# Performance work log

Hardware: AMD Instinct MI355X
Metric: run time of the kernel (lower is better)

Reference implementation:

```python
import jax, jax.numpy as jnp
import numpy as np

B, T, E = 512, 12, 1024   # batch, channels/seq, embed_dim
NH, HS = 8, 128           # num_heads, head_size (head_size=128 hard-coded in source)
H = NH * HS               # sLSTM hidden = 1024 (== E)


def _layer_norm(x, g, b, eps=1e-5):
    mu = x.mean(-1, keepdims=True)
    var = x.var(-1, keepdims=True)
    return (x - mu) * jax.lax.rsqrt(var + eps) * g + b


def _conv1d_same(x, w, b):
    # x: (B, C, L), w: (O, I, K) odd K, 'same' padding, stride 1
    k = w.shape[-1]
    p = (k - 1) // 2
    y = jax.lax.conv_general_dilated(x, w, (1,), [(p, p)],
                                     dimension_numbers=('NCH', 'OIH', 'NCH'))
    return y + b[None, :, None]


def setup_inputs():
    key = jax.random.key(0)
    ks = jax.random.split(key, 16)
    s = 0.02
    def nrm(k, shape, scale=s):
        return jax.random.normal(k, shape, jnp.float32) * scale
    return {
        'x': jax.random.normal(ks[0], (B, T, E), jnp.float32),
        'ln_g': jnp.ones((E,), jnp.float32), 'ln_b': jnp.zeros((E,), jnp.float32),
        'fc1_w': nrm(ks[1], (12, 12, 3)), 'fc1_b': jnp.zeros((12,), jnp.float32),
        'fc2_w': nrm(ks[2], (12, 12)), 'fc2_b': jnp.zeros((12,), jnp.float32),
        'conv1_w': nrm(ks[3], (48, 12, 3)), 'conv1_b': jnp.zeros((48,), jnp.float32),
        'conv2_w': nrm(ks[4], (12, 48, 3)), 'conv2_b': jnp.zeros((12,), jnp.float32),
        'xl_ln_g': jnp.ones((E,), jnp.float32), 'xl_ln_b': jnp.zeros((E,), jnp.float32),
        'Wg': nrm(ks[5], (E, 4 * H)), 'bg': jnp.zeros((4 * H,), jnp.float32),
        'Rg': nrm(ks[6], (NH, 4 * HS, HS)),
        'gn_g': jnp.ones((H,), jnp.float32), 'gn_b': jnp.zeros((H,), jnp.float32),
        'upl_w': nrm(ks[7], (H, H)), 'upl_b': jnp.zeros((H,), jnp.float32),
        'upr_w': nrm(ks[8], (H, H)), 'upr_b': jnp.zeros((H,), jnp.float32),
        'down_w': nrm(ks[9], (H, E)), 'down_b': jnp.zeros((E,), jnp.float32),
    }


def _slstm_block(x, xl_ln_g, xl_ln_b, Wg, bg, Rg, gn_g, gn_b,
                 upl_w, upl_b, upr_w, upr_b, down_w, down_b):
    # Stabilized multi-head sLSTM block: pre-LN -> sLSTM recurrence (exp i/f gates
    # with max-stabilizer m), per-head GroupNorm, gated up/down proj (proj_factor=1),
    # residual. Recurrent weights are block-diagonal per head (NH, 4*HS, HS).
    xn = _layer_norm(x, xl_ln_g, xl_ln_b)
    gx = jnp.einsum('bte,eg->btg', xn, Wg) + bg            # (B,T,4H) input gate pre-acts
    gx = jnp.swapaxes(gx, 0, 1)                            # (T,B,4H)

    def step(carry, g_t):
        h, c, n, m = carry                                 # each (B,NH,HS)
        rec = jnp.einsum('bnh,ngh->bng', h, Rg)            # (B,NH,4HS)
        g = g_t.reshape(g_t.shape[0], NH, 4 * HS) + rec
        z_, i_, f_, o_ = jnp.split(g, 4, axis=-1)
        z = jnp.tanh(z_)
        o = jax.nn.sigmoid(o_)
        m_new = jnp.maximum(f_ + m, i_)                    # log-space stabilizer
        i = jnp.exp(i_ - m_new)
        f = jnp.exp(f_ + m - m_new)
        c = f * c + i * z
        n = f * n + i
        h = o * (c / n)
        return (h, c, n, m_new), h

    zero = jnp.zeros((x.shape[0], NH, HS), x.dtype)
    _, hseq = jax.lax.scan(step, (zero, zero, zero, zero), gx)
    h = jnp.swapaxes(hseq, 0, 1)                           # (B,T,NH,HS)
    # GroupNorm(num_groups=NH) over each head's HS channels
    mu = h.mean(-1, keepdims=True)
    var = h.var(-1, keepdims=True)
    hn = (h - mu) * jax.lax.rsqrt(var + 1e-5)
    hn = hn.reshape(x.shape[0], x.shape[1], H) * gn_g + gn_b
    left = jax.nn.gelu(hn @ upl_w + upl_b, approximate=False)
    right = hn @ upr_w + upr_b
    return (left * right) @ down_w + down_b + x


def reference(x, ln_g, ln_b, fc1_w, fc1_b, fc2_w, fc2_b, conv1_w, conv1_b,
              conv2_w, conv2_b, xl_ln_g, xl_ln_b, Wg, bg, Rg, gn_g, gn_b,
              upl_w, upl_b, upr_w, upr_b, down_w, down_b):
    xn = _layer_norm(x, ln_g, ln_b)
    skip = xn
    xc = _conv1d_same(xn, fc1_w, fc1_b)                    # fc1: Conv1d(12,12,3,'same')
    x1 = jnp.einsum('bcl,oc->bol', xc, fc2_w) + fc2_b[None, :, None]  # fc2: 1x1 conv
    x1 = _slstm_block(x1, xl_ln_g, xl_ln_b, Wg, bg, Rg, gn_g, gn_b,
                      upl_w, upl_b, upr_w, upr_b, down_w, down_b)
    # dropout(0.2) is identity in eval mode
    y = jax.nn.silu(xc) * x1 + skip
    z = _conv1d_same(y, conv1_w, conv1_b)                  # 12 -> 48
    z = _layer_norm(jax.nn.gelu(z, approximate=False), ln_g, ln_b)
    z = _conv1d_same(z, conv2_w, conv2_b)                  # 48 -> 12
    return z + skip
```

## Files before the change

### kernel.cpp

```cpp
#include <hip/hip_runtime.h>
#include <math.h>


typedef short short8_t __attribute__((ext_vector_type(8)));
typedef float floatx4 __attribute__((ext_vector_type(4)));
typedef float float2_t __attribute__((ext_vector_type(2)));

typedef unsigned int u32;
typedef const __attribute__((address_space(1))) u32 gu32;
typedef __attribute__((address_space(3))) u32 lu32;

static __device__ __forceinline__ float b2f(unsigned short u) {
    unsigned v = ((unsigned)u) << 16;
    return __builtin_bit_cast(float, v);
}
static __device__ __forceinline__ unsigned short f2b(float f) {
    unsigned u = __builtin_bit_cast(unsigned, f);
    u += 0x7FFFu + ((u >> 16) & 1u);
    return (unsigned short)(u >> 16);
}
static __device__ __forceinline__ float2_t make2u(unsigned u) {
    float2_t r;
    r.x = __builtin_bit_cast(float, u << 16);
    r.y = __builtin_bit_cast(float, u & 0xFFFF0000u);
    return r;
}
static __device__ __forceinline__ u32 pack2(float a, float b) {
    return ((u32)f2b(b) << 16) | (u32)f2b(a);
}
static __device__ __forceinline__ float gelu_fast(float x) {
    float u = 0.7978845608f * x * (1.f + 0.044715f * x * x);
    u = fminf(fmaxf(u, -9.f), 9.f);
    return x * __builtin_amdgcn_rcpf(1.f + __expf(-2.f * u));
}


__global__ __launch_bounds__(256) void transpose_bf16_k(
    const float* __restrict__ src, unsigned short* __restrict__ dst, int K, int N)
{
    __shared__ unsigned short tl[32][33];
    const int n0 = blockIdx.x * 32, k0 = blockIdx.y * 32;
    const int tx = threadIdx.x & 31, ty = threadIdx.x >> 5;
#pragma unroll
    for (int r = 0; r < 4; r++) {
        int k = ty + r * 8;
        tl[tx][k] = f2b(src[(size_t)(k0 + k) * N + n0 + tx]);
    }
    __syncthreads();
#pragma unroll
    for (int r = 0; r < 4; r++) {
        int n = ty * 4 + r;
        dst[(size_t)(n0 + n) * K + k0 + tx] = tl[n][tx];
    }
}


template <int BF16OUT>
__global__ __launch_bounds__(256) void ln_kernel(
    const float* __restrict__ in, const float* __restrict__ g,
    const float* __restrict__ be, void* __restrict__ outp)
{
    const int row = blockIdx.x;
    const float* xr = in + (size_t)row * 1024;
    const int t = threadIdx.x;
    float v[4];
    float s = 0.f, ss = 0.f;
#pragma unroll
    for (int u = 0; u < 4; u++) {
        float q = xr[t + u * 256];
        v[u] = q; s += q; ss += q * q;
    }
#pragma unroll
    for (int off = 32; off >= 1; off >>= 1) {
        s += __shfl_xor(s, off);
        ss += __shfl_xor(ss, off);
    }
    __shared__ float red[8];
    const int wv = t >> 6, la = t & 63;
    if (la == 0) { red[wv] = s; red[4 + wv] = ss; }
    __syncthreads();
    s = red[0] + red[1] + red[2] + red[3];
    ss = red[4] + red[5] + red[6] + red[7];
    float mu = s * (1.f / 1024.f);
    float var = ss * (1.f / 1024.f) - mu * mu;
    float rs = rsqrtf(var + 1e-5f);
#pragma unroll
    for (int u = 0; u < 4; u++) {
        int i = t + u * 256;
        float yv = (v[u] - mu) * rs * g[i] + be[i];
        if (BF16OUT)
            ((unsigned short*)outp)[(size_t)row * 1024 + i] = f2b(yv);
        else
            ((float*)outp)[(size_t)row * 1024 + i] = yv;
    }
}


__global__ __launch_bounds__(256) void fc_kernel(
    const float* __restrict__ xn,
    const float* __restrict__ w1, const float* __restrict__ b1,
    const float* __restrict__ w2, const float* __restrict__ b2,
    float* __restrict__ xc, float* __restrict__ x1)
{
    const int t = threadIdx.x;
    const int gid = blockIdx.x * 256 + t;
    const int b = gid >> 10, l = gid & 1023;
    const float* xb = xn + (size_t)b * 12288;
    float inm[12], in0[12], inp[12];
#pragma unroll
    for (int ci = 0; ci < 12; ci++) {
        in0[ci] = xb[ci * 1024 + l];
        inm[ci] = (l > 0) ? xb[ci * 1024 + l - 1] : 0.f;
        inp[ci] = (l < 1023) ? xb[ci * 1024 + l + 1] : 0.f;
    }
    float xcv[12];
#pragma unroll
    for (int o = 0; o < 12; o++) {
        float a = b1[o];
#pragma unroll
        for (int ci = 0; ci < 12; ci++) {
            const float* wp = w1 + o * 36 + ci * 3;
            a += inm[ci] * wp[0] + in0[ci] * wp[1] + inp[ci] * wp[2];
        }
        xcv[o] = a;
        xc[(size_t)b * 12288 + o * 1024 + l] = a;
    }
#pragma unroll
    for (int o = 0; o < 12; o++) {
        float a = b2[o];
#pragma unroll
        for (int ci = 0; ci < 12; ci++) a += xcv[ci] * w2[o * 12 + ci];
        x1[(size_t)b * 12288 + o * 1024 + l] = a;
    }
}


template <int MODE>
__global__ __launch_bounds__(256) void gemm_kernel(
    const unsigned short* __restrict__ A, const unsigned short* __restrict__ BT,
    const float* __restrict__ bias, void* __restrict__ out,
    int M, int N, int K,
    const float* __restrict__ xc, const float* __restrict__ x1,
    const float* __restrict__ skip)
{
    __shared__ __align__(16) unsigned short sA[128 * 32];
    __shared__ __align__(16) unsigned short sB[128 * 32];
    const int t = threadIdx.x;
    const int m0 = blockIdx.y * 128;
    const int n0 = blockIdx.x * 128;
    const int w = t >> 6;
    const int lane = t & 63;
    const int wr = (w >> 1) * 64;
    const int wc = (w & 1) * 64;
    const int lrow = lane & 15;
    const int quad = lane >> 4;
    const int row_l = t >> 2;
    const int cs = (t & 3) * 8;

    const unsigned short* gA0 = A + (size_t)(m0 + row_l) * K + cs;
    const unsigned short* gA1 = A + (size_t)(m0 + row_l + 64) * K + cs;
    const unsigned short* gB0 = BT + (size_t)(n0 + row_l) * K + cs;
    const unsigned short* gB1 = BT + (size_t)(n0 + row_l + 64) * K + cs;
    unsigned short* lA0 = sA + w * 512;
    unsigned short* lA1 = sA + 2048 + w * 512;
    unsigned short* lB0 = sB + w * 512;
    unsigned short* lB1 = sB + 2048 + w * 512;

    floatx4 acc[4][4];
#pragma unroll
    for (int i = 0; i < 4; i++)
#pragma unroll
        for (int j = 0; j < 4; j++) acc[i][j] = (floatx4)0.f;

    for (int k0 = 0; k0 < K; k0 += 32) {
        __syncthreads();
        __builtin_amdgcn_global_load_lds((gu32*)(gA0 + k0), (lu32*)lA0, 16, 0, 0);
        __builtin_amdgcn_global_load_lds((gu32*)(gA1 + k0), (lu32*)lA1, 16, 0, 0);
        __builtin_amdgcn_global_load_lds((gu32*)(gB0 + k0), (lu32*)lB0, 16, 0, 0);
        __builtin_amdgcn_global_load_lds((gu32*)(gB1 + k0), (lu32*)lB1, 16, 0, 0);
        __syncthreads();
        short8_t af[4], bfr[4];
#pragma unroll
        for (int i = 0; i < 4; i++) {
            af[i] = *(const short8_t*)(sA + (wr + i * 16 + lrow) * 32 + quad * 8);
            bfr[i] = *(const short8_t*)(sB + (wc + i * 16 + lrow) * 32 + quad * 8);
        }
#pragma unroll
        for (int i = 0; i < 4; i++)
#pragma unroll
            for (int j = 0; j < 4; j++)
                acc[i][j] = __builtin_amdgcn_mfma_f32_16x16x32_bf16(
                    af[i], bfr[j], acc[i][j], 0, 0, 0);
    }

#pragma unroll
    for (int i = 0; i < 4; i++) {
#pragma unroll
        for (int j = 0; j < 4; j++) {
#pragma unroll
            for (int r = 0; r < 4; r++) {
                const int gm = m0 + wr + i * 16 + quad * 4 + r;
                const int gn = n0 + wc + j * 16 + lrow;
                const size_t idx = (size_t)gm * N + gn;
                float v = acc[i][j][r] + bias[gn];
                if (MODE == 0) {
                    ((unsigned short*)out)[idx] = f2b(v);
                } else {
                    float xcv = xc[idx];
                    float sig = xcv * __builtin_amdgcn_rcpf(1.f + __expf(-xcv));
                    ((unsigned short*)out)[idx] =
                        f2b(sig * (v + x1[idx]) + skip[idx]);
                }
            }
        }
    }
}


#define RECP 516
#define HBP  136

__global__ __launch_bounds__(1024, 1) void slstm_rec_kernel(
    const float* __restrict__ Rg,
    const unsigned short* __restrict__ gxb,
    const float* __restrict__ gn_g, const float* __restrict__ gn_b,
    unsigned short* __restrict__ hnb)
{
    __shared__ __align__(16) float sRec[16 * RECP];
    __shared__ __align__(16) unsigned short sHb[16 * HBP];
    const int head = blockIdx.x;
    const int b0 = blockIdx.y * 16;
    const int t = threadIdx.x;
    const int w = t >> 6;
    const int lane = t & 63;
    const int quad = lane >> 4;
    const int l16 = lane & 15;

    short8_t Bf[2][4];
    {
        const float* Rh = Rg + (size_t)head * 65536;
#pragma unroll
        for (int jt = 0; jt < 2; jt++)
#pragma unroll
            for (int kk = 0; kk < 4; kk++) {
                const float* src =
                    Rh + (size_t)(w * 32 + jt * 16 + l16) * 128 + kk * 32 + quad * 8;
                short8_t v;
#pragma unroll
                for (int j = 0; j < 8; j++) v[j] = (short)f2b(src[j]);
                Bf[jt][kk] = v;
            }
    }

    for (int i = t; i < 16 * HBP; i += 1024) sHb[i] = 0;

    const int la = lane;
    float c0 = 0.f, n0s = 0.f, m0 = 0.f;
    float c1 = 0.f, n1s = 0.f, m1 = 0.f;
    const float gg0 = gn_g[head * 128 + la];
    const float gg1 = gn_g[head * 128 + la + 64];
    const float gb0 = gn_b[head * 128 + la];
    const float gb1 = gn_b[head * 128 + la + 64];

    __syncthreads();

    for (int step = 0; step < 12; step++) {
        const unsigned short* gp =
            gxb + ((size_t)(b0 + w) * 12 + step) * 4096 + head * 512;
        float gz0 = b2f(gp[la]),       gz1 = b2f(gp[64 + la]);
        float gi0 = b2f(gp[128 + la]), gi1 = b2f(gp[192 + la]);
        float gf0 = b2f(gp[256 + la]), gf1 = b2f(gp[320 + la]);
        float go0 = b2f(gp[384 + la]), go1 = b2f(gp[448 + la]);

        short8_t Af[4];
#pragma unroll
        for (int kk = 0; kk < 4; kk++)
            Af[kk] = *(const short8_t*)(sHb + l16 * HBP + kk * 32 + quad * 8);
        floatx4 D0 = (floatx4)0.f, D1 = (floatx4)0.f;
#pragma unroll
        for (int kk = 0; kk < 4; kk++) {
            D0 = __builtin_amdgcn_mfma_f32_16x16x32_bf16(Af[kk], Bf[0][kk], D0, 0, 0, 0);
            D1 = __builtin_amdgcn_mfma_f32_16x16x32_bf16(Af[kk], Bf[1][kk], D1, 0, 0, 0);
        }
#pragma unroll
        for (int r = 0; r < 4; r++) {
            sRec[(quad * 4 + r) * RECP + w * 32 + l16] = D0[r];
            sRec[(quad * 4 + r) * RECP + w * 32 + 16 + l16] = D1[r];
        }
        __syncthreads();

        const float* rr = sRec + w * RECP;
        float zp0 = gz0 + rr[la],       zp1 = gz1 + rr[64 + la];
        float ip0 = gi0 + rr[128 + la], ip1 = gi1 + rr[192 + la];
        float fp0 = gf0 + rr[256 + la], fp1 = gf1 + rr[320 + la];
        float op0 = go0 + rr[384 + la], op1 = go1 + rr[448 + la];

        float e20 = __expf(-2.f * zp0), e21 = __expf(-2.f * zp1);
        float z0 = 2.f * __builtin_amdgcn_rcpf(1.f + e20) - 1.f;
        float z1 = 2.f * __builtin_amdgcn_rcpf(1.f + e21) - 1.f;
        float o0 = __builtin_amdgcn_rcpf(1.f + __expf(-op0));
        float o1 = __builtin_amdgcn_rcpf(1.f + __expf(-op1));
        float mn0 = fmaxf(fp0 + m0, ip0), mn1 = fmaxf(fp1 + m1, ip1);
        float ie0 = __expf(ip0 - mn0), ie1 = __expf(ip1 - mn1);
        float fe0 = __expf(fp0 + m0 - mn0), fe1 = __expf(fp1 + m1 - mn1);
        c0 = fe0 * c0 + ie0 * z0;  c1 = fe1 * c1 + ie1 * z1;
        n0s = fe0 * n0s + ie0;     n1s = fe1 * n1s + ie1;
        m0 = mn0;                  m1 = mn1;
        float h0 = o0 * c0 * __builtin_amdgcn_rcpf(n0s);
        float h1 = o1 * c1 * __builtin_amdgcn_rcpf(n1s);

        float s = h0 + h1, ss = h0 * h0 + h1 * h1;
#pragma unroll
        for (int off = 32; off >= 1; off >>= 1) {
            s += __shfl_xor(s, off);
            ss += __shfl_xor(ss, off);
        }
        float mu = s * (1.f / 128.f);
        float var = ss * (1.f / 128.f) - mu * mu;
        float rs = rsqrtf(var + 1e-5f);
        size_t base = ((size_t)(b0 + w) * 12 + step) * 1024 + head * 128;
        hnb[base + la] = f2b((h0 - mu) * rs * gg0 + gb0);
        hnb[base + la + 64] = f2b((h1 - mu) * rs * gg1 + gb1);

        sHb[w * HBP + la] = f2b(h0);
        sHb[w * HBP + la + 64] = f2b(h1);
        __syncthreads();
    }
}


__global__ __launch_bounds__(256) void gate_kernel(
    const unsigned short* __restrict__ lr, unsigned short* __restrict__ glr)
{
    u32 pi = blockIdx.x * 256 + threadIdx.x;
    u32 m = pi >> 9, c = pi & 511;
    const u32* row = (const u32*)(lr + (size_t)m * 2048);
    float2_t lf = make2u(row[c]);
    float2_t rt = make2u(row[512 + c]);
    ((u32*)glr)[pi] = pack2(gelu_fast(lf.x) * rt.x, gelu_fast(lf.y) * rt.y);
}


__global__ __launch_bounds__(512, 6) void tail_fused_kernel(
    const unsigned short* __restrict__ y, const float* __restrict__ skip,
    const float* __restrict__ w1, const float* __restrict__ b1,
    const float* __restrict__ w2, const float* __restrict__ b2,
    const float* __restrict__ lng, const float* __restrict__ lnb,
    float* __restrict__ out)
{
    __shared__ unsigned short sY[12][1026];
    __shared__ unsigned short sZ[12][1026];
    __shared__ float sMR[12][2];
    const int b = blockIdx.x;
    const int t = threadIdx.x;
    const int p = t;
    const size_t boff = (size_t)b * 12288;

    {
        const u32* gy = (const u32*)(y + boff);
#pragma unroll
        for (int ci = 0; ci < 12; ci++)
            ((u32*)&sY[ci][0])[t] = gy[ci * 512 + t];
    }
    const float lgA = lng[2 * t], lbA = lnb[2 * t];
    const float lgB = lng[2 * t + 1], lbB = lnb[2 * t + 1];
    __syncthreads();

    float2_t acc[12];
#pragma unroll
    for (int o = 0; o < 12; o++) { float bv = b2[o]; acc[o] = float2_t{bv, bv}; }

    for (int q = 0; q < 4; q++) {
        float2_t a1[12];
#pragma unroll
        for (int o = 0; o < 12; o++) {
            float bo = b1[q * 12 + o];
            a1[o] = float2_t{bo, bo};
        }
        for (int ci = 0; ci < 12; ci++) {
            float2_t v0 = float2_t{b2f(sY[ci][p]), b2f(sY[ci][p + 512])};
            float2_t vm = float2_t{(p > 0) ? b2f(sY[ci][p - 1]) : 0.f,
                                   b2f(sY[ci][p + 511])};
            float2_t vp = float2_t{b2f(sY[ci][p + 1]),
                                   (p < 511) ? b2f(sY[ci][p + 513]) : 0.f};
            const float* wp = w1 + ci * 3;
#pragma unroll
            for (int o = 0; o < 12; o++) {
                const float* wo = wp + (q * 12 + o) * 36;
                a1[o] += vm * wo[0] + v0 * wo[1] + vp * wo[2];
            }
        }
#pragma unroll
        for (int o = 0; o < 12; o++) {
            sZ[o][p] = f2b(gelu_fast(a1[o].x));
            sZ[o][p + 512] = f2b(gelu_fast(a1[o].y));
        }
        __syncthreads();

        {
            const int wv = t >> 6, la = t & 63;
#pragma unroll
            for (int j = 0; j < 2; j++) {
                const int ch = wv + j * 8;
                if (ch < 12) {
                    float s = 0.f, ss = 0.f;
#pragma unroll
                    for (int u = 0; u < 8; u++) {
                        float2_t v = make2u(((const u32*)&sZ[ch][0])[la + u * 64]);
                        s += v.x + v.y;
                        ss += v.x * v.x + v.y * v.y;
                    }
#pragma unroll
                    for (int off = 32; off >= 1; off >>= 1) {
                        s += __shfl_xor(s, off);
                        ss += __shfl_xor(ss, off);
                    }
                    if (la == 0) {
                        float mu = s * (1.f / 1024.f);
                        float var = ss * (1.f / 1024.f) - mu * mu;
                        sMR[ch][0] = mu;
                        sMR[ch][1] = rsqrtf(var + 1e-5f);
                    }
                }
            }
        }
        __syncthreads();

#pragma unroll
        for (int ch = 0; ch < 12; ch++) {
            const float mu = sMR[ch][0], rs = sMR[ch][1];
            float2_t f = make2u(((const u32*)&sZ[ch][0])[t]);
            f.x = (f.x - mu) * rs * lgA + lbA;
            f.y = (f.y - mu) * rs * lgB + lbB;
            ((u32*)&sZ[ch][0])[t] = pack2(f.x, f.y);
        }
        __syncthreads();

        for (int ci = 0; ci < 12; ci++) {
            float2_t z0 = float2_t{b2f(sZ[ci][p]), b2f(sZ[ci][p + 512])};
            float2_t zm = float2_t{(p > 0) ? b2f(sZ[ci][p - 1]) : 0.f,
                                   b2f(sZ[ci][p + 511])};
            float2_t zp = float2_t{b2f(sZ[ci][p + 1]),
                                   (p < 511) ? b2f(sZ[ci][p + 513]) : 0.f};
            const float* wp = w2 + (q * 12 + ci) * 3;
#pragma unroll
            for (int o = 0; o < 12; o++)
                acc[o] += zm * wp[o * 144] + z0 * wp[o * 144 + 1]
                        + zp * wp[o * 144 + 2];
        }
        __syncthreads();
    }

#pragma unroll
    for (int o = 0; o < 12; o++) {
        size_t i0 = boff + (size_t)o * 1024 + p;
        out[i0] = acc[o].x + skip[i0];
        out[i0 + 512] = acc[o].y + skip[i0 + 512];
    }
}


extern "C" void kernel_launch(void* const* d_in, const int* in_sizes, int n_in,
                              void* d_out, int out_size, void* d_ws, size_t ws_size,
                              hipStream_t stream)
{
    (void)in_sizes; (void)n_in; (void)out_size; (void)ws_size;
    const float* x      = (const float*)d_in[0];
    const float* ln_g   = (const float*)d_in[1];
    const float* ln_b   = (const float*)d_in[2];
    const float* fc1_w  = (const float*)d_in[3];
    const float* fc1_b  = (const float*)d_in[4];
    const float* fc2_w  = (const float*)d_in[5];
    const float* fc2_b  = (const float*)d_in[6];
    const float* conv1_w= (const float*)d_in[7];
    const float* conv1_b= (const float*)d_in[8];
    const float* conv2_w= (const float*)d_in[9];
    const float* conv2_b= (const float*)d_in[10];
    const float* xl_g   = (const float*)d_in[11];
    const float* xl_b   = (const float*)d_in[12];
    const float* Wg     = (const float*)d_in[13];
    const float* bg     = (const float*)d_in[14];
    const float* Rg     = (const float*)d_in[15];
    const float* gn_g   = (const float*)d_in[16];
    const float* gn_b   = (const float*)d_in[17];
    const float* upl_w  = (const float*)d_in[18];
    const float* upl_b  = (const float*)d_in[19];
    const float* upr_w  = (const float*)d_in[20];
    const float* upr_b  = (const float*)d_in[21];
    const float* down_w = (const float*)d_in[22];
    const float* down_b = (const float*)d_in[23];

    char* ws = (char*)d_ws;
    size_t off = 0;
    auto alloc = [&](size_t bytes) -> char* {
        char* p = ws + off;
        off = (off + bytes + 255) & ~(size_t)255;
        return p;
    };
    float* xn            = (float*)alloc(25165824);
    float* xc            = (float*)alloc(25165824);
    float* x1            = (float*)alloc(25165824);
    unsigned short* xn2b = (unsigned short*)alloc(12582912);
    unsigned short* gxb  = (unsigned short*)alloc(50331648);
    unsigned short* hnb  = (unsigned short*)alloc(12582912);
    unsigned short* lrb  = (unsigned short*)alloc(25165824);
    unsigned short* glrb = (unsigned short*)alloc(12582912);
    unsigned short* yb   = (unsigned short*)alloc(12582912);
    unsigned short* WgT  = (unsigned short*)alloc(8388608);
    unsigned short* WupT = (unsigned short*)alloc(4194304);
    unsigned short* WdT  = (unsigned short*)alloc(2097152);
    float* bup           = (float*)alloc(8192);

    transpose_bf16_k<<<dim3(128, 32), 256, 0, stream>>>(Wg, WgT, 1024, 4096);
    transpose_bf16_k<<<dim3(32, 32), 256, 0, stream>>>(upl_w, WupT, 1024, 1024);
    transpose_bf16_k<<<dim3(32, 32), 256, 0, stream>>>(upr_w, WupT + 1024 * 1024, 1024, 1024);
    transpose_bf16_k<<<dim3(32, 32), 256, 0, stream>>>(down_w, WdT, 1024, 1024);
    {
        hipMemcpyAsync(bup, upl_b, 4096, hipMemcpyDeviceToDevice, stream);
        hipMemcpyAsync(bup + 1024, upr_b, 4096, hipMemcpyDeviceToDevice, stream);
    }

    ln_kernel<0><<<6144, 256, 0, stream>>>(x, ln_g, ln_b, xn);
    fc_kernel<<<2048, 256, 0, stream>>>(xn, fc1_w, fc1_b, fc2_w, fc2_b, xc, x1);
    ln_kernel<1><<<6144, 256, 0, stream>>>(x1, xl_g, xl_b, xn2b);
    gemm_kernel<0><<<dim3(32, 48), 256, 0, stream>>>(
        xn2b, WgT, bg, gxb, 6144, 4096, 1024, nullptr, nullptr, nullptr);
    slstm_rec_kernel<<<dim3(8, 32), 1024, 0, stream>>>(Rg, gxb, gn_g, gn_b, hnb);
    gemm_kernel<0><<<dim3(16, 48), 256, 0, stream>>>(
        hnb, WupT, bup, lrb, 6144, 2048, 1024, nullptr, nullptr, nullptr);
    gate_kernel<<<12288, 256, 0, stream>>>(lrb, glrb);
    gemm_kernel<2><<<dim3(8, 48), 256, 0, stream>>>(
        glrb, WdT, down_b, yb, 6144, 1024, 1024, xc, x1, xn);
    tail_fused_kernel<<<512, 512, 0, stream>>>(
        yb, xn, conv1_w, conv1_b, conv2_w, conv2_b, ln_g, ln_b, (float*)d_out);
}
```

Before: 459.3 us.

## Fuse GELU gating into up-projection GEMM epilogue and LayerNorm into fc conv

```diff
diff --git a/kernel.cpp b/kernel.cpp
--- a/kernel.cpp
+++ b/kernel.cpp
@@ -36,7 +36,8 @@
 
 
 __global__ __launch_bounds__(256) void transpose_bf16_k(
-    const float* __restrict__ src, unsigned short* __restrict__ dst, int K, int N)
+    const float* __restrict__ src, unsigned short* __restrict__ dst,
+    int K, int N, int GS, int GO)
 {
     __shared__ unsigned short tl[32][33];
     const int n0 = blockIdx.x * 32, k0 = blockIdx.y * 32;
@@ -49,9 +50,19 @@
     __syncthreads();
 #pragma unroll
     for (int r = 0; r < 4; r++) {
-        int n = ty * 4 + r;
-        dst[(size_t)(n0 + n) * K + k0 + tx] = tl[n][tx];
-    }
+        int n = n0 + ty * 4 + r;
+        size_t row = (size_t)((n >> 4) * GS + GO + (n & 15));
+        dst[row * K + k0 + tx] = tl[ty * 4 + r][tx];
+    }
+}
+
+__global__ __launch_bounds__(256) void bias_ilv_kernel(
+    const float* __restrict__ bl, const float* __restrict__ br,
+    float* __restrict__ o)
+{
+    int i = blockIdx.x * 256 + threadIdx.x;
+    int grp = i >> 5, w = i & 31;
+    o[i] = (w < 16) ? bl[grp * 16 + w] : br[grp * 16 + (w - 16)];
 }
 
 
@@ -96,41 +107,106 @@
 }
 
 
-__global__ __launch_bounds__(256) void fc_kernel(
-    const float* __restrict__ xn,
+__global__ __launch_bounds__(512, 3) void ln_fc_kernel(
+    const float* __restrict__ x,
+    const float* __restrict__ g, const float* __restrict__ be,
     const float* __restrict__ w1, const float* __restrict__ b1,
     const float* __restrict__ w2, const float* __restrict__ b2,
-    float* __restrict__ xc, float* __restrict__ x1)
-{
+    float* __restrict__ xn, float* __restrict__ xc, float* __restrict__ x1)
+{
+    __shared__ float sX[12][1028];
+    __shared__ float sMR[12][2];
+    const int b = blockIdx.x;
     const int t = threadIdx.x;
-    const int gid = blockIdx.x * 256 + t;
-    const int b = gid >> 10, l = gid & 1023;
-    const float* xb = xn + (size_t)b * 12288;
-    float inm[12], in0[12], inp[12];
-#pragma unroll
+    const int p = t;
+    const size_t boff = (size_t)b * 12288;
+
+    if (t < 12) { sX[t][0] = 0.f; sX[t][1025] = 0.f; sX[t][1026] = 0.f; sX[t][1027] = 0.f; }
+    {
+        const float* gx = x + boff;
+#pragma unroll
+        for (int ci = 0; ci < 12; ci++) {
+            sX[ci][1 + p] = gx[ci * 1024 + p];
+            sX[ci][1 + p + 512] = gx[ci * 1024 + p + 512];
+        }
+    }
+    __syncthreads();
+
+    {
+        const int wv = t >> 6, la = t & 63;
+#pragma unroll
+        for (int j = 0; j < 2; j++) {
+            const int ch = wv + j * 8;
+            if (ch < 12) {
+                float s = 0.f, ss = 0.f;
+#pragma unroll
+                for (int u = 0; u < 16; u++) {
+                    float v = sX[ch][1 + la + u * 64];
+                    s += v; ss += v * v;
+                }
+#pragma unroll
+                for (int off = 32; off >= 1; off >>= 1) {
+                    s += __shfl_xor(s, off);
+                    ss += __shfl_xor(ss, off);
+                }
+                if (la == 0) {
+                    float mu = s * (1.f / 1024.f);
+                    float var = ss * (1.f / 1024.f) - mu * mu;
+                    sMR[ch][0] = mu;
+                    sMR[ch][1] = rsqrtf(var + 1e-5f);
+                }
+            }
+        }
+    }
+    __syncthreads();
+
+    const float gA = g[p], bA = be[p];
+    const float gB = g[p + 512], bB = be[p + 512];
+#pragma unroll
+    for (int ch = 0; ch < 12; ch++) {
+        const float mu = sMR[ch][0], rs = sMR[ch][1];
+        float v0 = (sX[ch][1 + p] - mu) * rs * gA + bA;
+        float v1 = (sX[ch][1 + p + 512] - mu) * rs * gB + bB;
+        sX[ch][1 + p] = v0;
+        sX[ch][1 + p + 512] = v1;
+        xn[boff + (size_t)ch * 1024 + p] = v0;
+        xn[boff + (size_t)ch * 1024 + p + 512] = v1;
+    }
+    __syncthreads();
+
+    float2_t a1[12];
+#pragma unroll
+    for (int o = 0; o < 12; o++) { float bv = b1[o]; a1[o] = float2_t{bv, bv}; }
     for (int ci = 0; ci < 12; ci++) {
-        in0[ci] = xb[ci * 1024 + l];
-        inm[ci] = (l > 0) ? xb[ci * 1024 + l - 1] : 0.f;
-        inp[ci] = (l < 1023) ? xb[ci * 1024 + l + 1] : 0.f;
-    }
-    float xcv[12];
+        float2_t vm = float2_t{sX[ci][p],     sX[ci][p + 512]};
+        float2_t v0 = float2_t{sX[ci][p + 1], sX[ci][p + 513]};
+        float2_t vp = float2_t{sX[ci][p + 2], sX[ci][p + 514]};
+        const float* wp = w1 + ci * 3;
+#pragma unroll
+        for (int o = 0; o < 12; o++) {
+            const float* wo = wp + o * 36;
+            a1[o] += vm * wo[0] + v0 * wo[1] + vp * wo[2];
+        }
+    }
 #pragma unroll
     for (int o = 0; o < 12; o++) {
-        float a = b1[o];
-#pragma unroll
-        for (int ci = 0; ci < 12; ci++) {
-            const float* wp = w1 + o * 36 + ci * 3;
-            a += inm[ci] * wp[0] + in0[ci] * wp[1] + inp[ci] * wp[2];
-        }
-        xcv[o] = a;
-        xc[(size_t)b * 12288 + o * 1024 + l] = a;
+        xc[boff + (size_t)o * 1024 + p] = a1[o].x;
+        xc[boff + (size_t)o * 1024 + p + 512] = a1[o].y;
+    }
+
+    float2_t a2[12];
+#pragma unroll
+    for (int o = 0; o < 12; o++) { float bv = b2[o]; a2[o] = float2_t{bv, bv}; }
+#pragma unroll
+    for (int ci = 0; ci < 12; ci++) {
+#pragma unroll
+        for (int o = 0; o < 12; o++)
+            a2[o] += a1[ci] * w2[o * 12 + ci];
     }
 #pragma unroll
     for (int o = 0; o < 12; o++) {
-        float a = b2[o];
-#pragma unroll
-        for (int ci = 0; ci < 12; ci++) a += xcv[ci] * w2[o * 12 + ci];
-        x1[(size_t)b * 12288 + o * 1024 + l] = a;
+        x1[boff + (size_t)o * 1024 + p] = a2[o].x;
+        x1[boff + (size_t)o * 1024 + p + 512] = a2[o].y;
     }
 }
 
@@ -193,23 +269,42 @@
                     af[i], bfr[j], acc[i][j], 0, 0, 0);
     }
 
-#pragma unroll
-    for (int i = 0; i < 4; i++) {
-#pragma unroll
-        for (int j = 0; j < 4; j++) {
-#pragma unroll
-            for (int r = 0; r < 4; r++) {
-                const int gm = m0 + wr + i * 16 + quad * 4 + r;
-                const int gn = n0 + wc + j * 16 + lrow;
-                const size_t idx = (size_t)gm * N + gn;
-                float v = acc[i][j][r] + bias[gn];
-                if (MODE == 0) {
-                    ((unsigned short*)out)[idx] = f2b(v);
-                } else {
-                    float xcv = xc[idx];
-                    float sig = xcv * __builtin_amdgcn_rcpf(1.f + __expf(-xcv));
-                    ((unsigned short*)out)[idx] =
-                        f2b(sig * (v + x1[idx]) + skip[idx]);
+    if (MODE == 3) {
+#pragma unroll
+        for (int i = 0; i < 4; i++) {
+#pragma unroll
+            for (int k = 0; k < 2; k++) {
+#pragma unroll
+                for (int r = 0; r < 4; r++) {
+                    const int gm = m0 + wr + i * 16 + quad * 4 + r;
+                    const int pl = n0 + wc + k * 32 + lrow;
+                    float lv = acc[i][2 * k][r] + bias[pl];
+                    float rv = acc[i][2 * k + 1][r] + bias[pl + 16];
+                    const int nlog = (pl >> 5) * 16 + lrow;
+                    ((unsigned short*)out)[(size_t)gm * (N >> 1) + nlog] =
+                        f2b(gelu_fast(lv) * rv);
+                }
+            }
+        }
+    } else {
+#pragma unroll
+        for (int i = 0; i < 4; i++) {
+#pragma unroll
+            for (int j = 0; j < 4; j++) {
+#pragma unroll
+                for (int r = 0; r < 4; r++) {
+                    const int gm = m0 + wr + i * 16 + quad * 4 + r;
+                    const int gn = n0 + wc + j * 16 + lrow;
+                    const size_t idx = (size_t)gm * N + gn;
+                    float v = acc[i][j][r] + bias[gn];
+                    if (MODE == 0) {
+                        ((unsigned short*)out)[idx] = f2b(v);
+                    } else {
+                        float xcv = xc[idx];
+                        float sig = xcv * __builtin_amdgcn_rcpf(1.f + __expf(-xcv));
+                        ((unsigned short*)out)[idx] =
+                            f2b(sig * (v + x1[idx]) + skip[idx]);
+                    }
                 }
             }
         }
@@ -326,18 +421,6 @@
         sHb[w * HBP + la + 64] = f2b(h1);
         __syncthreads();
     }
-}
-
-
-__global__ __launch_bounds__(256) void gate_kernel(
-    const unsigned short* __restrict__ lr, unsigned short* __restrict__ glr)
-{
-    u32 pi = blockIdx.x * 256 + threadIdx.x;
-    u32 m = pi >> 9, c = pi & 511;
-    const u32* row = (const u32*)(lr + (size_t)m * 2048);
-    float2_t lf = make2u(row[c]);
-    float2_t rt = make2u(row[512 + c]);
-    ((u32*)glr)[pi] = pack2(gelu_fast(lf.x) * rt.x, gelu_fast(lf.y) * rt.y);
 }
 
 
@@ -503,7 +586,6 @@
     unsigned short* xn2b = (unsigned short*)alloc(12582912);
     unsigned short* gxb  = (unsigned short*)alloc(50331648);
     unsigned short* hnb  = (unsigned short*)alloc(12582912);
-    unsigned short* lrb  = (unsigned short*)alloc(25165824);
     unsigned short* glrb = (unsigned short*)alloc(12582912);
     unsigned short* yb   = (unsigned short*)alloc(12582912);
     unsigned short* WgT  = (unsigned short*)alloc(8388608);
@@ -511,24 +593,20 @@
     unsigned short* WdT  = (unsigned short*)alloc(2097152);
     float* bup           = (float*)alloc(8192);
 
-    transpose_bf16_k<<<dim3(128, 32), 256, 0, stream>>>(Wg, WgT, 1024, 4096);
-    transpose_bf16_k<<<dim3(32, 32), 256, 0, stream>>>(upl_w, WupT, 1024, 1024);
-    transpose_bf16_k<<<dim3(32, 32), 256, 0, stream>>>(upr_w, WupT + 1024 * 1024, 1024, 1024);
-    transpose_bf16_k<<<dim3(32, 32), 256, 0, stream>>>(down_w, WdT, 1024, 1024);
-    {
-        hipMemcpyAsync(bup, upl_b, 4096, hipMemcpyDeviceToDevice, stream);
-        hipMemcpyAsync(bup + 1024, upr_b, 4096, hipMemcpyDeviceToDevice, stream);
-    }
-
-    ln_kernel<0><<<6144, 256, 0, stream>>>(x, ln_g, ln_b, xn);
-    fc_kernel<<<2048, 256, 0, stream>>>(xn, fc1_w, fc1_b, fc2_w, fc2_b, xc, x1);
+    transpose_bf16_k<<<dim3(128, 32), 256, 0, stream>>>(Wg, WgT, 1024, 4096, 16, 0);
+    transpose_bf16_k<<<dim3(32, 32), 256, 0, stream>>>(upl_w, WupT, 1024, 1024, 32, 0);
+    transpose_bf16_k<<<dim3(32, 32), 256, 0, stream>>>(upr_w, WupT, 1024, 1024, 32, 16);
+    transpose_bf16_k<<<dim3(32, 32), 256, 0, stream>>>(down_w, WdT, 1024, 1024, 16, 0);
+    bias_ilv_kernel<<<8, 256, 0, stream>>>(upl_b, upr_b, bup);
+
+    ln_fc_kernel<<<512, 512, 0, stream>>>(
+        x, ln_g, ln_b, fc1_w, fc1_b, fc2_w, fc2_b, xn, xc, x1);
     ln_kernel<1><<<6144, 256, 0, stream>>>(x1, xl_g, xl_b, xn2b);
     gemm_kernel<0><<<dim3(32, 48), 256, 0, stream>>>(
         xn2b, WgT, bg, gxb, 6144, 4096, 1024, nullptr, nullptr, nullptr);
     slstm_rec_kernel<<<dim3(8, 32), 1024, 0, stream>>>(Rg, gxb, gn_g, gn_b, hnb);
-    gemm_kernel<0><<<dim3(16, 48), 256, 0, stream>>>(
-        hnb, WupT, bup, lrb, 6144, 2048, 1024, nullptr, nullptr, nullptr);
-    gate_kernel<<<12288, 256, 0, stream>>>(lrb, glrb);
+    gemm_kernel<3><<<dim3(16, 48), 256, 0, stream>>>(
+        hnb, WupT, bup, glrb, 6144, 2048, 1024, nullptr, nullptr, nullptr);
     gemm_kernel<2><<<dim3(8, 48), 256, 0, stream>>>(
         glrb, WdT, down_b, yb, 6144, 1024, 1024, xc, x1, xn);
     tail_fused_kernel<<<512, 512, 0, stream>>>(
```

After: 450.2 us. -2.0%, faster.
